# Optimization experiments

Hardware: AMD Instinct MI355X
Metric: run time of the kernel (lower is better)

Reference implementation:

```python
import jax, jax.numpy as jnp
import numpy as np

D = 128      # d_model
H = 8        # n_heads
HD = D // H  # head_dim = 16
E = 256      # n_experts
R = 32       # kv_lora_rank
B, T = 4, 512
EPS = 1e-6


def _dense_init(k, fi, fo):
    s = float(1.0 / np.sqrt(fi))
    return jax.random.uniform(k, (fi, fo), minval=-s, maxval=s, dtype=jnp.float32)


def setup_inputs() -> dict:
    key = jax.random.key(0)
    ks = jax.random.split(key, 16)
    rng = np.random.RandomState(42)
    Q, _ = np.linalg.qr(rng.randn(D, D))
    glim = float(np.sqrt(6.0 / (D + D)))
    return {
        'x': jax.random.normal(ks[0], (B, T, D), dtype=jnp.float32),
        'g1': jnp.ones((D,), jnp.float32),
        'qW': _dense_init(ks[1], D, D), 'qb': jnp.zeros((D,), jnp.float32),
        'kdW': _dense_init(ks[2], D, R), 'kdb': jnp.zeros((R,), jnp.float32),
        'kuW': _dense_init(ks[3], R, 2 * D), 'kub': jnp.zeros((2 * D,), jnp.float32),
        'oW': _dense_init(ks[4], D, D), 'ob': jnp.zeros((D,), jnp.float32),
        'rot': jnp.asarray(Q, jnp.float32),
        'tq_scale': jnp.ones((D,), jnp.float32),
        's1W': _dense_init(ks[5], D, D), 's1b': jnp.zeros((D,), jnp.float32),
        's2W': _dense_init(ks[6], D, D), 's2b': jnp.zeros((D,), jnp.float32),
        'g2': jnp.ones((D,), jnp.float32),
        'gateW': _dense_init(ks[7], D, E), 'gateb': jnp.zeros((E,), jnp.float32),
        'expW': jax.random.uniform(ks[8], (E, D, D), minval=-glim, maxval=glim, dtype=jnp.float32),
        'm1W': _dense_init(ks[9], D, D), 'm1b': jnp.zeros((D,), jnp.float32),
        'm2W': _dense_init(ks[10], D, D), 'm2b': jnp.zeros((D,), jnp.float32),
    }


def _rmsnorm(x, g):
    return g * (x / jnp.sqrt(jnp.mean(x * x, axis=-1, keepdims=True) + EPS))


def _swiglu(x, w1, b1, w2, b2):
    gate = x @ w1 + b1
    return gate * jax.nn.sigmoid(gate) * (x @ w2 + b2)


def _mla(x, qW, qb, kdW, kdb, kuW, kub, oW, ob):
    b, t = x.shape[0], x.shape[1]
    q = (x @ qW + qb).reshape(b, t, H, HD)
    kv = ((x @ kdW + kdb) @ kuW + kub).reshape(b, t, H, 2 * HD)
    k, v = jnp.split(kv, 2, axis=-1)
    q = jax.nn.elu(q) + 1.0
    k = jax.nn.elu(k) + 1.0
    # linear attention: context[b,h,d,e] = sum_t k[b,t,h,d] v[b,t,h,e]
    context = jnp.einsum('bthd,bthe->bhde', k, v)
    out = jnp.einsum('bthd,bhde->bthe', q, context)
    k_sum = jnp.sum(k, axis=1)  # [b,h,d]
    z = 1.0 / (jnp.einsum('bthd,bhd->bth', q, k_sum) + EPS)
    out = out * z[..., None]
    return out.reshape(b, t, D) @ oW + ob


def _turbo_quant(x, rot, scale):
    x = x @ rot
    mag = jnp.sqrt(jnp.mean(x * x, axis=-1, keepdims=True) + EPS)
    phase = x / mag
    qp = jnp.clip(phase * 127.0, -127.0, 127.0) / 127.0
    phase = jax.lax.stop_gradient(qp - phase) + phase  # straight-through
    return phase * mag * scale


def _moe(h, gateW, gateb, expW, m1W, m1b, m2W, m2b):
    gate_scores = jax.nn.softmax(h @ gateW + gateb, axis=-1)  # [B,T,E]
    top_vals, top_idx = jax.lax.top_k(gate_scores, 2)
    top_w = top_vals / (jnp.sum(top_vals, axis=-1, keepdims=True) + EPS)
    # dense all-expert compute as in the original module
    eo = jnp.einsum('btd,edo->bteo', h, expW)  # [B,T,E,D]
    mask = jnp.sum(jax.nn.one_hot(top_idx, E, dtype=h.dtype) * top_w[..., None], axis=2)  # [B,T,E]
    wavg = jnp.einsum('bteo,bte->bto', eo, mask)
    wavg = _swiglu(wavg, m1W, m1b, m2W, m2b)
    diff_sq = jnp.square(eo - wavg[:, :, None, :])
    wvar = jnp.einsum('bteo,bte->bto', diff_sq, mask)
    consensus = jnp.exp(-jnp.mean(wvar, axis=-1))  # [B,T]
    return wavg, consensus


def reference(x, g1, qW, qb, kdW, kdb, kuW, kub, oW, ob, rot, tq_scale,
              s1W, s1b, s2W, s2b, g2, gateW, gateb, expW, m1W, m1b, m2W, m2b):
    attn_out = _turbo_quant(_mla(_rmsnorm(x, g1), qW, qb, kdW, kdb, kuW, kub, oW, ob), rot, tq_scale)
    x = x + _swiglu(attn_out, s1W, s1b, s2W, s2b)
    moe_out, consensus = _moe(_rmsnorm(x, g2), gateW, gateb, expW, m1W, m1b, m2W, m2b)
    return x + moe_out, consensus
```

## Files before the change

kernel.cpp:

```cpp
#include <hip/hip_runtime.h>
#include <hip/hip_bf16.h>
#include <math.h>

static constexpr int Dd   = 128;
static constexpr int NH   = 8;
static constexpr int HD   = 16;
static constexpr int NE   = 256;
static constexpr int RR   = 32;
static constexpr int BB   = 4;
static constexpr int TT   = 512;
static constexpr int NTOK = BB * TT;
static constexpr int TPB  = 4;
#define EPSF 1e-6f

__device__ __forceinline__ float elu1(float v) { return v > 0.f ? v + 1.f : expf(v); }
__device__ __forceinline__ float sigm(float v) { return 1.f / (1.f + expf(-v)); }

__global__ __launch_bounds__(512) void k_pre(
    const float* __restrict__ x, const float* __restrict__ g1,
    const float* __restrict__ qW, const float* __restrict__ qb,
    const float* __restrict__ kdW, const float* __restrict__ kdb,
    const float* __restrict__ kuW, const float* __restrict__ kub,
    float* __restrict__ qbuf, float* __restrict__ kvbuf,
    float* __restrict__ ctx, float* __restrict__ ksum, int* __restrict__ cnt) {
  const int tid = threadIdx.x;
  const int j = tid & 127, g = tid >> 7;
  const int lane = tid & 63;
  const int n0 = blockIdx.x * TPB;

  __shared__ float4 h1T[128];
  __shared__ float4 part[3][128];
  __shared__ float4 kpart[8][32];
  __shared__ float4 kdT[32];
  __shared__ float4 kupart[256];
  __shared__ float4 rtmp[2];

  if (blockIdx.x == 0) {
    for (int i = tid; i < 32 * 256; i += 512) ctx[i] = 0.f;
    ksum[tid] = 0.f;
    if (tid < 256) cnt[tid] = 0;
  }

  float xv[4];
  if (tid < 128) {
    float v[4];
#pragma unroll
    for (int t = 0; t < 4; t++) { xv[t] = x[(n0 + t) * Dd + j]; v[t] = xv[t] * xv[t]; }
#pragma unroll
    for (int o = 32; o > 0; o >>= 1) {
#pragma unroll
      for (int t = 0; t < 4; t++) v[t] += __shfl_xor(v[t], o, 64);
    }
    if (lane == 0) rtmp[tid >> 6] = make_float4(v[0], v[1], v[2], v[3]);
  }
  __syncthreads();
  if (tid < 128) {
    float g1j = g1[j];
#pragma unroll
    for (int t = 0; t < 4; t++) {
      float ss = ((const float*)&rtmp[0])[t] + ((const float*)&rtmp[1])[t];
      ((float*)&h1T[j])[t] = g1j * xv[t] * rsqrtf(ss * (1.f / 128.f) + EPSF);
    }
  }
  __syncthreads();

  {
    float a0 = 0, a1 = 0, a2 = 0, a3 = 0;
    const float* Wp = qW + (g * 32) * Dd + j;
#pragma unroll 16
    for (int i = 0; i < 32; i++) {
      float4 h4 = h1T[g * 32 + i];
      float w = Wp[i * Dd];
      a0 += h4.x * w; a1 += h4.y * w; a2 += h4.z * w; a3 += h4.w * w;
    }
    if (g) part[g - 1][j] = make_float4(a0, a1, a2, a3);
    __syncthreads();
    if (g == 0) {
      float4 p0 = part[0][j], p1 = part[1][j], p2 = part[2][j];
      float bb = qb[j];
      qbuf[(n0 + 0) * Dd + j] = elu1(a0 + p0.x + p1.x + p2.x + bb);
      qbuf[(n0 + 1) * Dd + j] = elu1(a1 + p0.y + p1.y + p2.y + bb);
      qbuf[(n0 + 2) * Dd + j] = elu1(a2 + p0.z + p1.z + p2.z + bb);
      qbuf[(n0 + 3) * Dd + j] = elu1(a3 + p0.w + p1.w + p2.w + bb);
    }
    __syncthreads();
  }

  if (tid < 256) {
    int col = tid & 31, ksp = tid >> 5;
    float a0 = 0, a1 = 0, a2 = 0, a3 = 0;
    const float* Wp = kdW + (ksp * 16) * RR + col;
#pragma unroll
    for (int i = 0; i < 16; i++) {
      float4 h4 = h1T[ksp * 16 + i];
      float w = Wp[i * RR];
      a0 += h4.x * w; a1 += h4.y * w; a2 += h4.z * w; a3 += h4.w * w;
    }
    kpart[ksp][col] = make_float4(a0, a1, a2, a3);
  }
  __syncthreads();
  if (tid < 32) {
    float bb = kdb[tid];
    float s0 = bb, s1 = bb, s2 = bb, s3 = bb;
#pragma unroll
    for (int k = 0; k < 8; k++) {
      float4 p = kpart[k][tid];
      s0 += p.x; s1 += p.y; s2 += p.z; s3 += p.w;
    }
    kdT[tid] = make_float4(s0, s1, s2, s3);
  }
  __syncthreads();

  {
    int col = tid & 255, kh = tid >> 8;
    float a0 = 0, a1 = 0, a2 = 0, a3 = 0;
    const float* Wp = kuW + (kh * 16) * 256 + col;
#pragma unroll
    for (int r = 0; r < 16; r++) {
      float4 k4 = kdT[kh * 16 + r];
      float w = Wp[r * 256];
      a0 += k4.x * w; a1 += k4.y * w; a2 += k4.z * w; a3 += k4.w * w;
    }
    if (kh) kupart[col] = make_float4(a0, a1, a2, a3);
    __syncthreads();
    if (!kh) {
      float4 p = kupart[col];
      float bb = kub[col];
      bool isk = (col & 31) < 16;
      float v0 = a0 + p.x + bb, v1 = a1 + p.y + bb, v2 = a2 + p.z + bb, v3 = a3 + p.w + bb;
      kvbuf[(n0 + 0) * 256 + col] = isk ? elu1(v0) : v0;
      kvbuf[(n0 + 1) * 256 + col] = isk ? elu1(v1) : v1;
      kvbuf[(n0 + 2) * 256 + col] = isk ? elu1(v2) : v2;
      kvbuf[(n0 + 3) * 256 + col] = isk ? elu1(v3) : v3;
    }
  }
}

__global__ __launch_bounds__(256) void k_ctx(const float* __restrict__ kv,
                                             float* __restrict__ ctx,
                                             float* __restrict__ ksum) {
  const int blk = blockIdx.x;
  const int bh = blk >> 3, c = blk & 7;
  const int b = bh >> 3, h = bh & 7;
  const int tid = threadIdx.x;
  const int d = tid >> 4, e = tid & 15;
  __shared__ float sh[64 * 32];
#pragma unroll
  for (int r = 0; r < 8; r++) {
    int lin = r * 256 + tid;
    int tok = lin >> 5, off = lin & 31;
    sh[lin] = kv[((b * TT + c * 64 + tok) * 256) + h * 32 + off];
  }
  __syncthreads();
  float acc = 0.f, ks = 0.f;
#pragma unroll 4
  for (int t = 0; t < 64; t++) {
    float kk = sh[t * 32 + d];
    acc += kk * sh[t * 32 + 16 + e];
    ks += kk;
  }
  atomicAdd(&ctx[bh * 256 + d * 16 + e], acc);
  if (e == 0) atomicAdd(&ksum[bh * 16 + d], ks);
}

__global__ __launch_bounds__(512) void k_mid(
    const float* __restrict__ x, const float* __restrict__ qbuf,
    const float* __restrict__ ctx, const float* __restrict__ ksum,
    const float* __restrict__ oW, const float* __restrict__ ob,
    const float* __restrict__ rot, const float* __restrict__ tqs,
    const float* __restrict__ s1W, const float* __restrict__ s1b,
    const float* __restrict__ s2W, const float* __restrict__ s2b,
    const float* __restrict__ g2, const float* __restrict__ gateW,
    const float* __restrict__ gateb,
    float* __restrict__ xnbuf, float* __restrict__ h2buf,
    float* __restrict__ gw, int* __restrict__ gidx, int* __restrict__ cnt) {
  const int tid = threadIdx.x;
  const int j = tid & 127, g = tid >> 7;
  const int lane = tid & 63;
  const int n0 = blockIdx.x * TPB;
  const int b = n0 >> 9;

  __shared__ float4 bufA[128], bufB[128];
  __shared__ float4 part[3][128];
  __shared__ float4 gpart[256];
  __shared__ float4 rtmp[2];
  __shared__ float wvS[4][4]; __shared__ int wiS[4][4];
  __shared__ float zS[4][4];

  ((float*)&bufA[j])[g] = qbuf[(n0 + g) * Dd + j];
  __syncthreads();

  if (tid < 128) {
    int h = j >> 4, e = j & 15;
    const float* cpt = ctx + (b * NH + h) * 256;
    const float* kpt = ksum + (b * NH + h) * 16;
    float num[4] = {0, 0, 0, 0}, den[4] = {0, 0, 0, 0};
#pragma unroll
    for (int d = 0; d < 16; d++) {
      float cx = cpt[d * 16 + e], ks = kpt[d];
      float4 q4 = bufA[h * 16 + d];
      num[0] += q4.x * cx; num[1] += q4.y * cx; num[2] += q4.z * cx; num[3] += q4.w * cx;
      den[0] += q4.x * ks; den[1] += q4.y * ks; den[2] += q4.z * ks; den[3] += q4.w * ks;
    }
#pragma unroll
    for (int t = 0; t < 4; t++) ((float*)&bufB[j])[t] = num[t] / (den[t] + EPSF);
  }
  __syncthreads();

  {
    float a0 = 0, a1 = 0, a2 = 0, a3 = 0;
    const float* Wp = oW + (g * 32) * Dd + j;
#pragma unroll 16
    for (int i = 0; i < 32; i++) {
      float4 h4 = bufB[g * 32 + i];
      float w = Wp[i * Dd];
      a0 += h4.x * w; a1 += h4.y * w; a2 += h4.z * w; a3 += h4.w * w;
    }
    if (g) part[g - 1][j] = make_float4(a0, a1, a2, a3);
    __syncthreads();
    if (g == 0) {
      float4 p0 = part[0][j], p1 = part[1][j], p2 = part[2][j];
      float bb = ob[j];
      bufA[j] = make_float4(a0 + p0.x + p1.x + p2.x + bb, a1 + p0.y + p1.y + p2.y + bb,
                            a2 + p0.z + p1.z + p2.z + bb, a3 + p0.w + p1.w + p2.w + bb);
    }
    __syncthreads();
  }

  {
    float a0 = 0, a1 = 0, a2 = 0, a3 = 0;
    const float* Wp = rot + (g * 32) * Dd + j;
#pragma unroll 16
    for (int i = 0; i < 32; i++) {
      float4 h4 = bufA[g * 32 + i];
      float w = Wp[i * Dd];
      a0 += h4.x * w; a1 += h4.y * w; a2 += h4.z * w; a3 += h4.w * w;
    }
    if (g) part[g - 1][j] = make_float4(a0, a1, a2, a3);
    __syncthreads();
    float tot[4];
    if (g == 0) {
      float4 p0 = part[0][j], p1 = part[1][j], p2 = part[2][j];
      tot[0] = a0 + p0.x + p1.x + p2.x; tot[1] = a1 + p0.y + p1.y + p2.y;
      tot[2] = a2 + p0.z + p1.z + p2.z; tot[3] = a3 + p0.w + p1.w + p2.w;
      float v[4];
#pragma unroll
      for (int t = 0; t < 4; t++) v[t] = tot[t] * tot[t];
#pragma unroll
      for (int o = 32; o > 0; o >>= 1) {
#pragma unroll
        for (int t = 0; t < 4; t++) v[t] += __shfl_xor(v[t], o, 64);
      }
      if (lane == 0) rtmp[tid >> 6] = make_float4(v[0], v[1], v[2], v[3]);
    }
    __syncthreads();
    if (g == 0) {
      float scj = tqs[j];
#pragma unroll
      for (int t = 0; t < 4; t++) {
        float ss = ((const float*)&rtmp[0])[t] + ((const float*)&rtmp[1])[t];
        float mag = sqrtf(ss * (1.f / 128.f) + EPSF);
        float ph = tot[t] / mag;
        float p127 = fminf(fmaxf(ph * 127.f, -127.f), 127.f);
        ((float*)&bufB[j])[t] = (p127 * (1.f / 127.f)) * mag * scj;
      }
    }
    __syncthreads();
  }

  {
    float a0 = 0, a1 = 0, a2 = 0, a3 = 0;
    const float* Wp = (g < 2 ? s1W : s2W) + ((g & 1) * 64) * Dd + j;
#pragma unroll 16
    for (int i = 0; i < 64; i++) {
      float4 h4 = bufB[(g & 1) * 64 + i];
      float w = Wp[i * Dd];
      a0 += h4.x * w; a1 += h4.y * w; a2 += h4.z * w; a3 += h4.w * w;
    }
    if (g) part[g - 1][j] = make_float4(a0, a1, a2, a3);
    __syncthreads();
    float xn[4];
    if (g == 0) {
      float b1 = s1b[j], b2 = s2b[j];
      float4 p0 = part[0][j], p1 = part[1][j], p2 = part[2][j];
      float gv[4], uv[4];
      gv[0] = a0 + p0.x + b1; gv[1] = a1 + p0.y + b1;
      gv[2] = a2 + p0.z + b1; gv[3] = a3 + p0.w + b1;
      uv[0] = p1.x + p2.x + b2; uv[1] = p1.y + p2.y + b2;
      uv[2] = p1.z + p2.z + b2; uv[3] = p1.w + p2.w + b2;
      float v[4];
#pragma unroll
      for (int t = 0; t < 4; t++) {
        xn[t] = x[(n0 + t) * Dd + j] + gv[t] * sigm(gv[t]) * uv[t];
        xnbuf[(n0 + t) * Dd + j] = xn[t];
        v[t] = xn[t] * xn[t];
      }
#pragma unroll
      for (int o = 32; o > 0; o >>= 1) {
#pragma unroll
        for (int t = 0; t < 4; t++) v[t] += __shfl_xor(v[t], o, 64);
      }
      if (lane == 0) rtmp[tid >> 6] = make_float4(v[0], v[1], v[2], v[3]);
    }
    __syncthreads();
    if (g == 0) {
      float g2j = g2[j];
#pragma unroll
      for (int t = 0; t < 4; t++) {
        float ss = ((const float*)&rtmp[0])[t] + ((const float*)&rtmp[1])[t];
        float h2v = g2j * xn[t] * rsqrtf(ss * (1.f / 128.f) + EPSF);
        ((float*)&bufA[j])[t] = h2v;
        h2buf[(n0 + t) * Dd + j] = h2v;
      }
    }
    __syncthreads();
  }

  float val[4];
  {
    int col = tid & 255, kh = tid >> 8;
    float a0 = 0, a1 = 0, a2 = 0, a3 = 0;
    const float* Wp = gateW + (kh * 64) * NE + col;
#pragma unroll 16
    for (int i = 0; i < 64; i++) {
      float4 h4 = bufA[kh * 64 + i];
      float w = Wp[i * NE];
      a0 += h4.x * w; a1 += h4.y * w; a2 += h4.z * w; a3 += h4.w * w;
    }
    if (kh) gpart[col] = make_float4(a0, a1, a2, a3);
    __syncthreads();
    if (!kh) {
      float4 p = gpart[col];
      float bb = gateb[col];
      val[0] = a0 + p.x + bb; val[1] = a1 + p.y + bb;
      val[2] = a2 + p.z + bb; val[3] = a3 + p.w + bb;
    }
  }
  __syncthreads();

  float m1[4]; int i1[4];
  {
    if (tid < 256) {
      float bv[4]; int bi[4];
#pragma unroll
      for (int t = 0; t < 4; t++) { bv[t] = val[t]; bi[t] = tid; }
#pragma unroll
      for (int o = 32; o > 0; o >>= 1) {
#pragma unroll
        for (int t = 0; t < 4; t++) {
          float wv = __shfl_xor(bv[t], o, 64);
          int wi = __shfl_xor(bi[t], o, 64);
          if (wv > bv[t] || (wv == bv[t] && wi < bi[t])) { bv[t] = wv; bi[t] = wi; }
        }
      }
      if (lane == 0) {
#pragma unroll
        for (int t = 0; t < 4; t++) { wvS[tid >> 6][t] = bv[t]; wiS[tid >> 6][t] = bi[t]; }
      }
    }
    __syncthreads();
    if (tid < 256) {
#pragma unroll
      for (int t = 0; t < 4; t++) {
        m1[t] = wvS[0][t]; i1[t] = wiS[0][t];
#pragma unroll
        for (int w = 1; w < 4; w++) {
          float cv = wvS[w][t]; int ci = wiS[w][t];
          if (cv > m1[t] || (cv == m1[t] && ci < i1[t])) { m1[t] = cv; i1[t] = ci; }
        }
      }
    }
    __syncthreads();
  }
  float m2[4]; int i2[4];
  {
    if (tid < 256) {
      float bv[4]; int bi[4];
#pragma unroll
      for (int t = 0; t < 4; t++) {
        bv[t] = (tid == i1[t]) ? -INFINITY : val[t];
        bi[t] = tid;
      }
#pragma unroll
      for (int o = 32; o > 0; o >>= 1) {
#pragma unroll
        for (int t = 0; t < 4; t++) {
          float wv = __shfl_xor(bv[t], o, 64);
          int wi = __shfl_xor(bi[t], o, 64);
          if (wv > bv[t] || (wv == bv[t] && wi < bi[t])) { bv[t] = wv; bi[t] = wi; }
        }
      }
      if (lane == 0) {
#pragma unroll
        for (int t = 0; t < 4; t++) { wvS[tid >> 6][t] = bv[t]; wiS[tid >> 6][t] = bi[t]; }
      }
    }
    __syncthreads();
    if (tid < 256) {
#pragma unroll
      for (int t = 0; t < 4; t++) {
        m2[t] = wvS[0][t]; i2[t] = wiS[0][t];
#pragma unroll
        for (int w = 1; w < 4; w++) {
          float cv = wvS[w][t]; int ci = wiS[w][t];
          if (cv > m2[t] || (cv == m2[t] && ci < i2[t])) { m2[t] = cv; i2[t] = ci; }
        }
      }
    }
    __syncthreads();
  }
  {
    if (tid < 256) {
      float v[4];
#pragma unroll
      for (int t = 0; t < 4; t++) v[t] = expf(val[t] - m1[t]);
#pragma unroll
      for (int o = 32; o > 0; o >>= 1) {
#pragma unroll
        for (int t = 0; t < 4; t++) v[t] += __shfl_xor(v[t], o, 64);
      }
      if (lane == 0) {
#pragma unroll
        for (int t = 0; t < 4; t++) zS[tid >> 6][t] = v[t];
      }
    }
    __syncthreads();
  }
  if (tid < 4) {
    int t = tid;
    float Z = zS[0][t] + zS[1][t] + zS[2][t] + zS[3][t];
    float p1 = 1.f / Z;
    float p2 = expf(m2[t] - m1[t]) / Z;
    float s = p1 + p2 + EPSF;
    gidx[(n0 + t) * 2 + 0] = i1[t];
    gidx[(n0 + t) * 2 + 1] = i2[t];
    gw[(n0 + t) * 2 + 0] = p1 / s;
    gw[(n0 + t) * 2 + 1] = p2 / s;
    atomicAdd(&cnt[i1[t]], 1);
    atomicAdd(&cnt[i2[t]], 1);
  }
}

__global__ __launch_bounds__(256) void k_route(const int* __restrict__ cnt,
                                               const int* __restrict__ gidx,
                                               int* __restrict__ offb,
                                               int* __restrict__ slottok,
                                               int* __restrict__ tokslot) {
  const int tid = threadIdx.x;
  __shared__ int sc[256];
  __shared__ int lcur[256];
  int c = cnt[tid];
  sc[tid] = c;
  __syncthreads();
  for (int o = 1; o < 256; o <<= 1) {
    int a = (tid >= o) ? sc[tid - o] : 0;
    __syncthreads();
    sc[tid] += a;
    __syncthreads();
  }
  int excl = sc[tid] - c;
  offb[tid] = excl;
  lcur[tid] = excl;
  __syncthreads();
  for (int base = 0; base < NTOK; base += 256) {
    int tok = base + tid;
    int e1 = gidx[tok * 2], e2 = gidx[tok * 2 + 1];
    int s1 = atomicAdd(&lcur[e1], 1);
    tokslot[tok * 2] = s1; slottok[s1] = tok;
    int s2 = atomicAdd(&lcur[e2], 1);
    tokslot[tok * 2 + 1] = s2; slottok[s2] = tok;
  }
}

__global__ __launch_bounds__(512) void k_exp(const float* __restrict__ h2buf,
                                             const int* __restrict__ slottok,
                                             const int* __restrict__ cnt,
                                             const int* __restrict__ offb,
                                             const float* __restrict__ expW,
                                             float* __restrict__ ybuf) {
  const int e = blockIdx.x;
  const int n = cnt[e];
  if (n == 0) return;
  const int base = offb[e];
  const int tid = threadIdx.x;
  const int j = tid & 127, g = tid >> 7;
  __shared__ __align__(16) float hT[128 * 20];
  const float* Wp = expW + (size_t)e * Dd * Dd + j;
  for (int t0 = 0; t0 < n; t0 += 16) {
    int m = n - t0; if (m > 16) m = 16;
    __syncthreads();
    for (int tt = g; tt < m; tt += 4) {
      int tok = slottok[base + t0 + tt];
      hT[j * 20 + tt] = h2buf[tok * Dd + j];
    }
    __syncthreads();
    float acc[4] = {0, 0, 0, 0};
#pragma unroll 8
    for (int i = 0; i < 128; i++) {
      float w = Wp[i * Dd];
      float4 h4 = *(const float4*)&hT[i * 20 + g * 4];
      acc[0] += h4.x * w; acc[1] += h4.y * w; acc[2] += h4.z * w; acc[3] += h4.w * w;
    }
#pragma unroll
    for (int k = 0; k < 4; k++) {
      int tt = g * 4 + k;
      if (tt < m) ybuf[(size_t)(base + t0 + tt) * Dd + j] = acc[k];
    }
  }
}

__global__ __launch_bounds__(512) void k_post(
    const float* __restrict__ xnbuf, const float* __restrict__ ybuf,
    const int* __restrict__ tokslot, const float* __restrict__ gw,
    const float* __restrict__ m1W, const float* __restrict__ m1b,
    const float* __restrict__ m2W, const float* __restrict__ m2b,
    float* __restrict__ out) {
  const int tid = threadIdx.x;
  const int j = tid & 127, g = tid >> 7;
  const int lane = tid & 63;
  const int n0 = blockIdx.x * TPB;

  __shared__ float4 y1T[128], y2T[128], inT[128], sT[128];
  __shared__ float4 part[3][128];
  __shared__ float4 rtmp[2];
  __shared__ int sSlot[4][2];
  __shared__ float sWt[4][2];

  if (tid < 4) {
    sSlot[tid][0] = tokslot[(n0 + tid) * 2];
    sSlot[tid][1] = tokslot[(n0 + tid) * 2 + 1];
    sWt[tid][0] = gw[(n0 + tid) * 2];
    sWt[tid][1] = gw[(n0 + tid) * 2 + 1];
  }
  __syncthreads();

  {
    float y1 = ybuf[(size_t)sSlot[g][0] * Dd + j];
    float y2 = ybuf[(size_t)sSlot[g][1] * Dd + j];
    ((float*)&y1T[j])[g] = y1;
    ((float*)&y2T[j])[g] = y2;
    ((float*)&inT[j])[g] = sWt[g][0] * y1 + sWt[g][1] * y2;
  }
  __syncthreads();

  {
    float a0 = 0, a1 = 0, a2 = 0, a3 = 0;
    const float* Wp = (g < 2 ? m1W : m2W) + ((g & 1) * 64) * Dd + j;
#pragma unroll 16
    for (int i = 0; i < 64; i++) {
      float4 h4 = inT[(g & 1) * 64 + i];
      float w = Wp[i * Dd];
      a0 += h4.x * w; a1 += h4.y * w; a2 += h4.z * w; a3 += h4.w * w;
    }
    if (g) part[g - 1][j] = make_float4(a0, a1, a2, a3);
    __syncthreads();
    if (g == 0) {
      float b1 = m1b[j], b2 = m2b[j];
      float4 p0 = part[0][j], p1 = part[1][j], p2 = part[2][j];
      float gv[4], uv[4];
      gv[0] = a0 + p0.x + b1; gv[1] = a1 + p0.y + b1;
      gv[2] = a2 + p0.z + b1; gv[3] = a3 + p0.w + b1;
      uv[0] = p1.x + p2.x + b2; uv[1] = p1.y + p2.y + b2;
      uv[2] = p1.z + p2.z + b2; uv[3] = p1.w + p2.w + b2;
#pragma unroll
      for (int t = 0; t < 4; t++) {
        float sv = gv[t] * sigm(gv[t]) * uv[t];
        ((float*)&sT[j])[t] = sv;
        out[(n0 + t) * Dd + j] = xnbuf[(n0 + t) * Dd + j] + sv;
      }
    }
    __syncthreads();
  }

  if (tid < 128) {
    float v[4];
#pragma unroll
    for (int t = 0; t < 4; t++) {
      float sv = ((const float*)&sT[j])[t];
      float d1 = ((const float*)&y1T[j])[t] - sv;
      float d2 = ((const float*)&y2T[j])[t] - sv;
      v[t] = sWt[t][0] * d1 * d1 + sWt[t][1] * d2 * d2;
    }
#pragma unroll
    for (int o = 32; o > 0; o >>= 1) {
#pragma unroll
      for (int t = 0; t < 4; t++) v[t] += __shfl_xor(v[t], o, 64);
    }
    if (lane == 0) rtmp[tid >> 6] = make_float4(v[0], v[1], v[2], v[3]);
  }
  __syncthreads();
  if (tid < 4) {
    float s = ((const float*)&rtmp[0])[tid] + ((const float*)&rtmp[1])[tid];
    out[NTOK * Dd + n0 + tid] = expf(-s * (1.f / 128.f));
  }
}

extern "C" void kernel_launch(void* const* d_in, const int* in_sizes, int n_in,
                              void* d_out, int out_size, void* d_ws, size_t ws_size,
                              hipStream_t stream) {
  const float* x   = (const float*)d_in[0];
  const float* g1  = (const float*)d_in[1];
  const float* qW  = (const float*)d_in[2];
  const float* qb  = (const float*)d_in[3];
  const float* kdW = (const float*)d_in[4];
  const float* kdb = (const float*)d_in[5];
  const float* kuW = (const float*)d_in[6];
  const float* kub = (const float*)d_in[7];
  const float* oW  = (const float*)d_in[8];
  const float* ob  = (const float*)d_in[9];
  const float* rot = (const float*)d_in[10];
  const float* tqs = (const float*)d_in[11];
  const float* s1W = (const float*)d_in[12];
  const float* s1b = (const float*)d_in[13];
  const float* s2W = (const float*)d_in[14];
  const float* s2b = (const float*)d_in[15];
  const float* g2  = (const float*)d_in[16];
  const float* gW  = (const float*)d_in[17];
  const float* gb  = (const float*)d_in[18];
  const float* eW  = (const float*)d_in[19];
  const float* m1W = (const float*)d_in[20];
  const float* m1b = (const float*)d_in[21];
  const float* m2W = (const float*)d_in[22];
  const float* m2b = (const float*)d_in[23];
  float* out = (float*)d_out;
  float* ws  = (float*)d_ws;

  float* qbuf  = ws;
  float* kvbuf = ws + 262144;
  float* ybuf  = ws;
  float* ctx   = ws + 786432;
  float* ksum  = ctx + 8192;
  float* h2buf = ksum + 512;
  float* xnbuf = h2buf + 262144;
  float* gw    = xnbuf + 262144;
  int*   gidx    = (int*)(gw + 4096);
  int*   cnt     = gidx + 4096;
  int*   offb    = cnt + 256;
  int*   slottok = offb + 256;
  int*   tokslot = slottok + 4096;

  k_pre<<<NTOK / TPB, 512, 0, stream>>>(x, g1, qW, qb, kdW, kdb, kuW, kub,
                                        qbuf, kvbuf, ctx, ksum, cnt);
  k_ctx<<<256, 256, 0, stream>>>(kvbuf, ctx, ksum);
  k_mid<<<NTOK / TPB, 512, 0, stream>>>(x, qbuf, ctx, ksum, oW, ob, rot, tqs,
                                        s1W, s1b, s2W, s2b, g2, gW, gb,
                                        xnbuf, h2buf, gw, gidx, cnt);
  k_route<<<1, 256, 0, stream>>>(cnt, gidx, offb, slottok, tokslot);
  k_exp<<<NE, 512, 0, stream>>>(h2buf, slottok, cnt, offb, eW, ybuf);
  k_post<<<NTOK / TPB, 512, 0, stream>>>(xnbuf, ybuf, tokslot, gw,
                                         m1W, m1b, m2W, m2b, out);
}
```

Before: 172.1 us.

## Fold weight products, defer RMSNorm scaling, and replace routing kernel with fixed slots

A new init kernel precomputes oW·rot and kdW·kuW, plus their folded biases, on every call. This lets k_pre run a single x→kv projection alongside the q projection in a 768-thread block, and lets k_mid drop the separate rotation matmul. RMSNorm scaling is applied after the matmuls instead of before, and the turbo-quant step is reduced to an equivalent clamp. The single-block k_route prefix-scan kernel is removed: tokens go into fixed 256-slot buckets per expert through atomics in k_mid. The risk is that an expert receiving more than 256 tokens has its excess silently clamped, and the extra init kernel adds a small cost.

```diff
diff --git a/kernel.cpp b/kernel.cpp
--- a/kernel.cpp
+++ b/kernel.cpp
@@ -11,41 +11,80 @@
 static constexpr int TT   = 512;
 static constexpr int NTOK = BB * TT;
 static constexpr int TPB  = 4;
+static constexpr int SLOTS = 256;
 #define EPSF 1e-6f
 
 __device__ __forceinline__ float elu1(float v) { return v > 0.f ? v + 1.f : expf(v); }
 __device__ __forceinline__ float sigm(float v) { return 1.f / (1.f + expf(-v)); }
 
-__global__ __launch_bounds__(512) void k_pre(
+__global__ __launch_bounds__(256) void k_init(
+    const float* __restrict__ oW, const float* __restrict__ ob,
+    const float* __restrict__ rot,
+    const float* __restrict__ kdW, const float* __restrict__ kdb,
+    const float* __restrict__ kuW, const float* __restrict__ kub,
+    float* __restrict__ oR, float* __restrict__ bR,
+    float* __restrict__ kvW, float* __restrict__ bkv,
+    float* __restrict__ ctx, float* __restrict__ ksum, int* __restrict__ cnt) {
+  const int blk = blockIdx.x, tid = threadIdx.x;
+  if (blk < 64) {
+    int row = blk * 2 + (tid >> 7), col = tid & 127;
+    const float* ow = oW + row * 128;
+    float acc = 0.f;
+#pragma unroll 8
+    for (int k = 0; k < 128; k++) acc += ow[k] * rot[k * 128 + col];
+    oR[row * 128 + col] = acc;
+  } else if (blk == 64) {
+    if (tid < 128) {
+      float acc = 0.f;
+#pragma unroll 8
+      for (int k = 0; k < 128; k++) acc += ob[k] * rot[k * 128 + tid];
+      bR[tid] = acc;
+    }
+    {
+      float acc = kub[tid];
+#pragma unroll
+      for (int k = 0; k < 32; k++) acc += kdb[k] * kuW[k * 256 + tid];
+      bkv[tid] = acc;
+    }
+    for (int i = tid; i < 32 * 256; i += 256) ctx[i] = 0.f;
+    for (int i = tid; i < 512; i += 256) ksum[i] = 0.f;
+    cnt[tid] = 0;
+  } else {
+    int idx = (blk - 65) * 256 + tid;
+    int row = idx >> 8, col = idx & 255;
+    const float* kw = kdW + row * 32;
+    float acc = 0.f;
+#pragma unroll
+    for (int k = 0; k < 32; k++) acc += kw[k] * kuW[k * 256 + col];
+    kvW[row * 256 + col] = acc;
+  }
+}
+
+__global__ __launch_bounds__(768) void k_pre(
     const float* __restrict__ x, const float* __restrict__ g1,
     const float* __restrict__ qW, const float* __restrict__ qb,
-    const float* __restrict__ kdW, const float* __restrict__ kdb,
-    const float* __restrict__ kuW, const float* __restrict__ kub,
-    float* __restrict__ qbuf, float* __restrict__ kvbuf,
-    float* __restrict__ ctx, float* __restrict__ ksum, int* __restrict__ cnt) {
+    const float* __restrict__ kvW, const float* __restrict__ bkv,
+    float* __restrict__ qbuf, float* __restrict__ kvbuf) {
   const int tid = threadIdx.x;
-  const int j = tid & 127, g = tid >> 7;
   const int lane = tid & 63;
   const int n0 = blockIdx.x * TPB;
 
-  __shared__ float4 h1T[128];
-  __shared__ float4 part[3][128];
-  __shared__ float4 kpart[8][32];
-  __shared__ float4 kdT[32];
-  __shared__ float4 kupart[256];
+  __shared__ float4 xgT[128];
+  __shared__ float4 qpart[128];
+  __shared__ float4 kvpart[256];
   __shared__ float4 rtmp[2];
 
-  if (blockIdx.x == 0) {
-    for (int i = tid; i < 32 * 256; i += 512) ctx[i] = 0.f;
-    ksum[tid] = 0.f;
-    if (tid < 256) cnt[tid] = 0;
-  }
-
-  float xv[4];
   if (tid < 128) {
-    float v[4];
-#pragma unroll
-    for (int t = 0; t < 4; t++) { xv[t] = x[(n0 + t) * Dd + j]; v[t] = xv[t] * xv[t]; }
+    int j = tid;
+    float g1j = g1[j];
+    float v[4], xg[4];
+#pragma unroll
+    for (int t = 0; t < 4; t++) {
+      float xv = x[(n0 + t) * Dd + j];
+      v[t] = xv * xv;
+      xg[t] = xv * g1j;
+    }
+    xgT[j] = make_float4(xg[0], xg[1], xg[2], xg[3]);
 #pragma unroll
     for (int o = 32; o > 0; o >>= 1) {
 #pragma unroll
@@ -54,84 +93,60 @@
     if (lane == 0) rtmp[tid >> 6] = make_float4(v[0], v[1], v[2], v[3]);
   }
   __syncthreads();
-  if (tid < 128) {
-    float g1j = g1[j];
+
+  float a0 = 0, a1 = 0, a2 = 0, a3 = 0;
+  const bool isq = tid < 256;
+  int j, kh;
+  if (isq) {
+    j = tid & 127; kh = tid >> 7;
+    const float* Wp = qW + (kh * 64) * Dd + j;
+    const float4* hb = xgT + kh * 64;
+#pragma unroll 16
+    for (int i = 0; i < 64; i++) {
+      float4 h4 = hb[i];
+      float w = Wp[i * Dd];
+      a0 += h4.x * w; a1 += h4.y * w; a2 += h4.z * w; a3 += h4.w * w;
+    }
+    if (kh) qpart[j] = make_float4(a0, a1, a2, a3);
+  } else {
+    int u = tid - 256;
+    j = u & 255; kh = u >> 8;
+    const float* Wp = kvW + (kh * 64) * 256 + j;
+    const float4* hb = xgT + kh * 64;
+#pragma unroll 16
+    for (int i = 0; i < 64; i++) {
+      float4 h4 = hb[i];
+      float w = Wp[i * 256];
+      a0 += h4.x * w; a1 += h4.y * w; a2 += h4.z * w; a3 += h4.w * w;
+    }
+    if (kh) kvpart[j] = make_float4(a0, a1, a2, a3);
+  }
+  __syncthreads();
+
+  if (kh == 0) {
+    float r[4];
 #pragma unroll
     for (int t = 0; t < 4; t++) {
       float ss = ((const float*)&rtmp[0])[t] + ((const float*)&rtmp[1])[t];
-      ((float*)&h1T[j])[t] = g1j * xv[t] * rsqrtf(ss * (1.f / 128.f) + EPSF);
-    }
-  }
-  __syncthreads();
-
-  {
-    float a0 = 0, a1 = 0, a2 = 0, a3 = 0;
-    const float* Wp = qW + (g * 32) * Dd + j;
-#pragma unroll 16
-    for (int i = 0; i < 32; i++) {
-      float4 h4 = h1T[g * 32 + i];
-      float w = Wp[i * Dd];
-      a0 += h4.x * w; a1 += h4.y * w; a2 += h4.z * w; a3 += h4.w * w;
-    }
-    if (g) part[g - 1][j] = make_float4(a0, a1, a2, a3);
-    __syncthreads();
-    if (g == 0) {
-      float4 p0 = part[0][j], p1 = part[1][j], p2 = part[2][j];
+      r[t] = rsqrtf(ss * (1.f / 128.f) + EPSF);
+    }
+    if (isq) {
+      float4 p = qpart[j];
       float bb = qb[j];
-      qbuf[(n0 + 0) * Dd + j] = elu1(a0 + p0.x + p1.x + p2.x + bb);
-      qbuf[(n0 + 1) * Dd + j] = elu1(a1 + p0.y + p1.y + p2.y + bb);
-      qbuf[(n0 + 2) * Dd + j] = elu1(a2 + p0.z + p1.z + p2.z + bb);
-      qbuf[(n0 + 3) * Dd + j] = elu1(a3 + p0.w + p1.w + p2.w + bb);
-    }
-    __syncthreads();
-  }
-
-  if (tid < 256) {
-    int col = tid & 31, ksp = tid >> 5;
-    float a0 = 0, a1 = 0, a2 = 0, a3 = 0;
-    const float* Wp = kdW + (ksp * 16) * RR + col;
-#pragma unroll
-    for (int i = 0; i < 16; i++) {
-      float4 h4 = h1T[ksp * 16 + i];
-      float w = Wp[i * RR];
-      a0 += h4.x * w; a1 += h4.y * w; a2 += h4.z * w; a3 += h4.w * w;
-    }
-    kpart[ksp][col] = make_float4(a0, a1, a2, a3);
-  }
-  __syncthreads();
-  if (tid < 32) {
-    float bb = kdb[tid];
-    float s0 = bb, s1 = bb, s2 = bb, s3 = bb;
-#pragma unroll
-    for (int k = 0; k < 8; k++) {
-      float4 p = kpart[k][tid];
-      s0 += p.x; s1 += p.y; s2 += p.z; s3 += p.w;
-    }
-    kdT[tid] = make_float4(s0, s1, s2, s3);
-  }
-  __syncthreads();
-
-  {
-    int col = tid & 255, kh = tid >> 8;
-    float a0 = 0, a1 = 0, a2 = 0, a3 = 0;
-    const float* Wp = kuW + (kh * 16) * 256 + col;
-#pragma unroll
-    for (int r = 0; r < 16; r++) {
-      float4 k4 = kdT[kh * 16 + r];
-      float w = Wp[r * 256];
-      a0 += k4.x * w; a1 += k4.y * w; a2 += k4.z * w; a3 += k4.w * w;
-    }
-    if (kh) kupart[col] = make_float4(a0, a1, a2, a3);
-    __syncthreads();
-    if (!kh) {
-      float4 p = kupart[col];
-      float bb = kub[col];
-      bool isk = (col & 31) < 16;
-      float v0 = a0 + p.x + bb, v1 = a1 + p.y + bb, v2 = a2 + p.z + bb, v3 = a3 + p.w + bb;
-      kvbuf[(n0 + 0) * 256 + col] = isk ? elu1(v0) : v0;
-      kvbuf[(n0 + 1) * 256 + col] = isk ? elu1(v1) : v1;
-      kvbuf[(n0 + 2) * 256 + col] = isk ? elu1(v2) : v2;
-      kvbuf[(n0 + 3) * 256 + col] = isk ? elu1(v3) : v3;
+      qbuf[(n0 + 0) * Dd + j] = elu1((a0 + p.x) * r[0] + bb);
+      qbuf[(n0 + 1) * Dd + j] = elu1((a1 + p.y) * r[1] + bb);
+      qbuf[(n0 + 2) * Dd + j] = elu1((a2 + p.z) * r[2] + bb);
+      qbuf[(n0 + 3) * Dd + j] = elu1((a3 + p.w) * r[3] + bb);
+    } else {
+      float4 p = kvpart[j];
+      float bb = bkv[j];
+      bool isk = (j & 31) < 16;
+      float v0 = (a0 + p.x) * r[0] + bb, v1 = (a1 + p.y) * r[1] + bb;
+      float v2 = (a2 + p.z) * r[2] + bb, v3 = (a3 + p.w) * r[3] + bb;
+      kvbuf[(n0 + 0) * 256 + j] = isk ? elu1(v0) : v0;
+      kvbuf[(n0 + 1) * 256 + j] = isk ? elu1(v1) : v1;
+      kvbuf[(n0 + 2) * 256 + j] = isk ? elu1(v2) : v2;
+      kvbuf[(n0 + 3) * 256 + j] = isk ? elu1(v3) : v3;
     }
   }
 }
@@ -166,14 +181,15 @@
 __global__ __launch_bounds__(512) void k_mid(
     const float* __restrict__ x, const float* __restrict__ qbuf,
     const float* __restrict__ ctx, const float* __restrict__ ksum,
-    const float* __restrict__ oW, const float* __restrict__ ob,
-    const float* __restrict__ rot, const float* __restrict__ tqs,
+    const float* __restrict__ oR, const float* __restrict__ bR,
+    const float* __restrict__ tqs,
     const float* __restrict__ s1W, const float* __restrict__ s1b,
     const float* __restrict__ s2W, const float* __restrict__ s2b,
     const float* __restrict__ g2, const float* __restrict__ gateW,
     const float* __restrict__ gateb,
     float* __restrict__ xnbuf, float* __restrict__ h2buf,
-    float* __restrict__ gw, int* __restrict__ gidx, int* __restrict__ cnt) {
+    float* __restrict__ gw, int* __restrict__ tokslot,
+    int* __restrict__ slottok, int* __restrict__ cnt) {
   const int tid = threadIdx.x;
   const int j = tid & 127, g = tid >> 7;
   const int lane = tid & 63;
@@ -187,6 +203,12 @@
   __shared__ float wvS[4][4]; __shared__ int wiS[4][4];
   __shared__ float zS[4][4];
 
+  float xres[4];
+  if (tid < 128) {
+#pragma unroll
+    for (int t = 0; t < 4; t++) xres[t] = x[(n0 + t) * Dd + j];
+  }
+
   ((float*)&bufA[j])[g] = qbuf[(n0 + g) * Dd + j];
   __syncthreads();
 
@@ -209,7 +231,7 @@
 
   {
     float a0 = 0, a1 = 0, a2 = 0, a3 = 0;
-    const float* Wp = oW + (g * 32) * Dd + j;
+    const float* Wp = oR + (g * 32) * Dd + j;
 #pragma unroll 16
     for (int i = 0; i < 32; i++) {
       float4 h4 = bufB[g * 32 + i];
@@ -218,31 +240,12 @@
     }
     if (g) part[g - 1][j] = make_float4(a0, a1, a2, a3);
     __syncthreads();
-    if (g == 0) {
-      float4 p0 = part[0][j], p1 = part[1][j], p2 = part[2][j];
-      float bb = ob[j];
-      bufA[j] = make_float4(a0 + p0.x + p1.x + p2.x + bb, a1 + p0.y + p1.y + p2.y + bb,
-                            a2 + p0.z + p1.z + p2.z + bb, a3 + p0.w + p1.w + p2.w + bb);
-    }
-    __syncthreads();
-  }
-
-  {
-    float a0 = 0, a1 = 0, a2 = 0, a3 = 0;
-    const float* Wp = rot + (g * 32) * Dd + j;
-#pragma unroll 16
-    for (int i = 0; i < 32; i++) {
-      float4 h4 = bufA[g * 32 + i];
-      float w = Wp[i * Dd];
-      a0 += h4.x * w; a1 += h4.y * w; a2 += h4.z * w; a3 += h4.w * w;
-    }
-    if (g) part[g - 1][j] = make_float4(a0, a1, a2, a3);
-    __syncthreads();
     float tot[4];
     if (g == 0) {
       float4 p0 = part[0][j], p1 = part[1][j], p2 = part[2][j];
-      tot[0] = a0 + p0.x + p1.x + p2.x; tot[1] = a1 + p0.y + p1.y + p2.y;
-      tot[2] = a2 + p0.z + p1.z + p2.z; tot[3] = a3 + p0.w + p1.w + p2.w;
+      float bb = bR[j];
+      tot[0] = a0 + p0.x + p1.x + p2.x + bb; tot[1] = a1 + p0.y + p1.y + p2.y + bb;
+      tot[2] = a2 + p0.z + p1.z + p2.z + bb; tot[3] = a3 + p0.w + p1.w + p2.w + bb;
       float v[4];
 #pragma unroll
       for (int t = 0; t < 4; t++) v[t] = tot[t] * tot[t];
@@ -260,9 +263,8 @@
       for (int t = 0; t < 4; t++) {
         float ss = ((const float*)&rtmp[0])[t] + ((const float*)&rtmp[1])[t];
         float mag = sqrtf(ss * (1.f / 128.f) + EPSF);
-        float ph = tot[t] / mag;
-        float p127 = fminf(fmaxf(ph * 127.f, -127.f), 127.f);
-        ((float*)&bufB[j])[t] = (p127 * (1.f / 127.f)) * mag * scj;
+        float zc = fminf(fmaxf(tot[t], -mag), mag);
+        ((float*)&bufA[j])[t] = zc * scj;
       }
     }
     __syncthreads();
@@ -273,26 +275,26 @@
     const float* Wp = (g < 2 ? s1W : s2W) + ((g & 1) * 64) * Dd + j;
 #pragma unroll 16
     for (int i = 0; i < 64; i++) {
-      float4 h4 = bufB[(g & 1) * 64 + i];
+      float4 h4 = bufA[(g & 1) * 64 + i];
       float w = Wp[i * Dd];
       a0 += h4.x * w; a1 += h4.y * w; a2 += h4.z * w; a3 += h4.w * w;
     }
     if (g) part[g - 1][j] = make_float4(a0, a1, a2, a3);
     __syncthreads();
-    float xn[4];
     if (g == 0) {
       float b1 = s1b[j], b2 = s2b[j];
       float4 p0 = part[0][j], p1 = part[1][j], p2 = part[2][j];
-      float gv[4], uv[4];
+      float gv[4], uv[4], xn[4], v[4];
       gv[0] = a0 + p0.x + b1; gv[1] = a1 + p0.y + b1;
       gv[2] = a2 + p0.z + b1; gv[3] = a3 + p0.w + b1;
       uv[0] = p1.x + p2.x + b2; uv[1] = p1.y + p2.y + b2;
       uv[2] = p1.z + p2.z + b2; uv[3] = p1.w + p2.w + b2;
-      float v[4];
+      float g2j = g2[j];
 #pragma unroll
       for (int t = 0; t < 4; t++) {
-        xn[t] = x[(n0 + t) * Dd + j] + gv[t] * sigm(gv[t]) * uv[t];
+        xn[t] = xres[t] + gv[t] * sigm(gv[t]) * uv[t];
         xnbuf[(n0 + t) * Dd + j] = xn[t];
+        ((float*)&bufB[j])[t] = g2j * xn[t];
         v[t] = xn[t] * xn[t];
       }
 #pragma unroll
@@ -303,37 +305,37 @@
       if (lane == 0) rtmp[tid >> 6] = make_float4(v[0], v[1], v[2], v[3]);
     }
     __syncthreads();
-    if (g == 0) {
-      float g2j = g2[j];
-#pragma unroll
-      for (int t = 0; t < 4; t++) {
-        float ss = ((const float*)&rtmp[0])[t] + ((const float*)&rtmp[1])[t];
-        float h2v = g2j * xn[t] * rsqrtf(ss * (1.f / 128.f) + EPSF);
-        ((float*)&bufA[j])[t] = h2v;
-        h2buf[(n0 + t) * Dd + j] = h2v;
-      }
-    }
-    __syncthreads();
   }
 
   float val[4];
+  float r2[4];
   {
     int col = tid & 255, kh = tid >> 8;
     float a0 = 0, a1 = 0, a2 = 0, a3 = 0;
     const float* Wp = gateW + (kh * 64) * NE + col;
 #pragma unroll 16
     for (int i = 0; i < 64; i++) {
-      float4 h4 = bufA[kh * 64 + i];
+      float4 h4 = bufB[kh * 64 + i];
       float w = Wp[i * NE];
       a0 += h4.x * w; a1 += h4.y * w; a2 += h4.z * w; a3 += h4.w * w;
     }
     if (kh) gpart[col] = make_float4(a0, a1, a2, a3);
     __syncthreads();
+#pragma unroll
+    for (int t = 0; t < 4; t++) {
+      float ss = ((const float*)&rtmp[0])[t] + ((const float*)&rtmp[1])[t];
+      r2[t] = rsqrtf(ss * (1.f / 128.f) + EPSF);
+    }
     if (!kh) {
       float4 p = gpart[col];
       float bb = gateb[col];
-      val[0] = a0 + p.x + bb; val[1] = a1 + p.y + bb;
-      val[2] = a2 + p.z + bb; val[3] = a3 + p.w + bb;
+      val[0] = (a0 + p.x) * r2[0] + bb; val[1] = (a1 + p.y) * r2[1] + bb;
+      val[2] = (a2 + p.z) * r2[2] + bb; val[3] = (a3 + p.w) * r2[3] + bb;
+    }
+    if (tid < 128) {
+#pragma unroll
+      for (int t = 0; t < 4; t++)
+        h2buf[(n0 + t) * Dd + j] = ((const float*)&bufB[j])[t] * r2[t];
     }
   }
   __syncthreads();
@@ -427,61 +429,30 @@
     __syncthreads();
   }
   if (tid < 4) {
-    int t = tid;
+    int t = tid, tok = n0 + t;
     float Z = zS[0][t] + zS[1][t] + zS[2][t] + zS[3][t];
     float p1 = 1.f / Z;
     float p2 = expf(m2[t] - m1[t]) / Z;
     float s = p1 + p2 + EPSF;
-    gidx[(n0 + t) * 2 + 0] = i1[t];
-    gidx[(n0 + t) * 2 + 1] = i2[t];
-    gw[(n0 + t) * 2 + 0] = p1 / s;
-    gw[(n0 + t) * 2 + 1] = p2 / s;
-    atomicAdd(&cnt[i1[t]], 1);
-    atomicAdd(&cnt[i2[t]], 1);
-  }
-}
-
-__global__ __launch_bounds__(256) void k_route(const int* __restrict__ cnt,
-                                               const int* __restrict__ gidx,
-                                               int* __restrict__ offb,
-                                               int* __restrict__ slottok,
-                                               int* __restrict__ tokslot) {
-  const int tid = threadIdx.x;
-  __shared__ int sc[256];
-  __shared__ int lcur[256];
-  int c = cnt[tid];
-  sc[tid] = c;
-  __syncthreads();
-  for (int o = 1; o < 256; o <<= 1) {
-    int a = (tid >= o) ? sc[tid - o] : 0;
-    __syncthreads();
-    sc[tid] += a;
-    __syncthreads();
-  }
-  int excl = sc[tid] - c;
-  offb[tid] = excl;
-  lcur[tid] = excl;
-  __syncthreads();
-  for (int base = 0; base < NTOK; base += 256) {
-    int tok = base + tid;
-    int e1 = gidx[tok * 2], e2 = gidx[tok * 2 + 1];
-    int s1 = atomicAdd(&lcur[e1], 1);
-    tokslot[tok * 2] = s1; slottok[s1] = tok;
-    int s2 = atomicAdd(&lcur[e2], 1);
-    tokslot[tok * 2 + 1] = s2; slottok[s2] = tok;
+    int e1 = i1[t], e2 = i2[t];
+    int s1 = atomicAdd(&cnt[e1], 1); if (s1 > SLOTS - 1) s1 = SLOTS - 1;
+    int s2 = atomicAdd(&cnt[e2], 1); if (s2 > SLOTS - 1) s2 = SLOTS - 1;
+    int sl1 = e1 * SLOTS + s1, sl2 = e2 * SLOTS + s2;
+    slottok[sl1] = tok; slottok[sl2] = tok;
+    tokslot[tok * 2] = sl1; tokslot[tok * 2 + 1] = sl2;
+    gw[tok * 2] = p1 / s; gw[tok * 2 + 1] = p2 / s;
   }
 }
 
 __global__ __launch_bounds__(512) void k_exp(const float* __restrict__ h2buf,
                                              const int* __restrict__ slottok,
                                              const int* __restrict__ cnt,
-                                             const int* __restrict__ offb,
                                              const float* __restrict__ expW,
                                              float* __restrict__ ybuf) {
   const int e = blockIdx.x;
-  const int n = cnt[e];
+  int n = cnt[e]; if (n > SLOTS) n = SLOTS;
   if (n == 0) return;
-  const int base = offb[e];
+  const int base = e * SLOTS;
   const int tid = threadIdx.x;
   const int j = tid & 127, g = tid >> 7;
   __shared__ __align__(16) float hT[128 * 20];
@@ -625,28 +596,30 @@
   float* out = (float*)d_out;
   float* ws  = (float*)d_ws;
 
-  float* qbuf  = ws;
-  float* kvbuf = ws + 262144;
-  float* ybuf  = ws;
-  float* ctx   = ws + 786432;
-  float* ksum  = ctx + 8192;
-  float* h2buf = ksum + 512;
-  float* xnbuf = h2buf + 262144;
-  float* gw    = xnbuf + 262144;
-  int*   gidx    = (int*)(gw + 4096);
-  int*   cnt     = gidx + 4096;
-  int*   offb    = cnt + 256;
-  int*   slottok = offb + 256;
-  int*   tokslot = slottok + 4096;
-
-  k_pre<<<NTOK / TPB, 512, 0, stream>>>(x, g1, qW, qb, kdW, kdb, kuW, kub,
-                                        qbuf, kvbuf, ctx, ksum, cnt);
+  float* qbuf   = ws;
+  float* kvbuf  = ws + 262144;
+  float* ctx    = ws + 786432;
+  float* ksum   = ws + 794624;
+  float* h2buf  = ws + 795136;
+  float* xnbuf  = ws + 1057280;
+  float* gw     = ws + 1319424;
+  float* oRb    = ws + 1323520;
+  float* bRb    = ws + 1339904;
+  float* kvW    = ws + 1340032;
+  float* bkv    = ws + 1372800;
+  int*   cnt     = (int*)(ws + 1373056);
+  int*   tokslot = (int*)(ws + 1373312);
+  int*   slottok = (int*)(ws + 1377408);
+  float* ybuf   = ws + 1442944;
+
+  k_init<<<193, 256, 0, stream>>>(oW, ob, rot, kdW, kdb, kuW, kub,
+                                  oRb, bRb, kvW, bkv, ctx, ksum, cnt);
+  k_pre<<<NTOK / TPB, 768, 0, stream>>>(x, g1, qW, qb, kvW, bkv, qbuf, kvbuf);
   k_ctx<<<256, 256, 0, stream>>>(kvbuf, ctx, ksum);
-  k_mid<<<NTOK / TPB, 512, 0, stream>>>(x, qbuf, ctx, ksum, oW, ob, rot, tqs,
+  k_mid<<<NTOK / TPB, 512, 0, stream>>>(x, qbuf, ctx, ksum, oRb, bRb, tqs,
                                         s1W, s1b, s2W, s2b, g2, gW, gb,
-                                        xnbuf, h2buf, gw, gidx, cnt);
-  k_route<<<1, 256, 0, stream>>>(cnt, gidx, offb, slottok, tokslot);
-  k_exp<<<NE, 512, 0, stream>>>(h2buf, slottok, cnt, offb, eW, ybuf);
+                                        xnbuf, h2buf, gw, tokslot, slottok, cnt);
+  k_exp<<<NE, 512, 0, stream>>>(h2buf, slottok, cnt, eW, ybuf);
   k_post<<<NTOK / TPB, 512, 0, stream>>>(xnbuf, ybuf, tokslot, gw,
                                          m1W, m1b, m2W, m2b, out);
 }
```

Result: faster. 168.5 us (-2.1%).
